# Optimization experiments

Hardware: AMD Instinct MI355X
Metric: run time of the kernel (lower is better)

Reference implementation:

```python
import jax, jax.numpy as jnp
import numpy as np
import math

D_MODEL = 1024
NUM_HEADS = 16
D_K = D_MODEL // NUM_HEADS
THETA = 10000.0
BATCH = 2
SEQ = 2048


def _trunc_normal(key, shape, std):
    # truncated normal in [-3std, 3std], matching torch.nn.init.trunc_normal_
    return jax.random.truncated_normal(key, -3.0, 3.0, shape, jnp.float32) * std


def setup_inputs() -> dict:
    key = jax.random.key(0)
    kx, kq, kk, kv, ko = jax.random.split(key, 5)
    std = math.sqrt(2.0 / (D_MODEL + D_MODEL))
    return {
        "x": jax.random.normal(kx, (BATCH, SEQ, D_MODEL), jnp.float32),
        "Wq": _trunc_normal(kq, (D_MODEL, D_MODEL), std),
        "Wk": _trunc_normal(kk, (D_MODEL, D_MODEL), std),
        "Wv": _trunc_normal(kv, (D_MODEL, D_MODEL), std),
        "Wo": _trunc_normal(ko, (D_MODEL, D_MODEL), std),
    }


def _apply_rope(t):
    # t: [B, H, S, d_k]; positions = arange(S)
    S = t.shape[-2]
    inv_freq = 1.0 / THETA ** (jnp.arange(0, D_K, 2, dtype=jnp.float32) / D_K)
    ang = jnp.arange(S, dtype=jnp.float32)[:, None] * inv_freq[None, :]  # [S, d_k/2]
    cos, sin = jnp.cos(ang), jnp.sin(ang)
    t1 = t[..., ::2]
    t2 = t[..., 1::2]
    r1 = t1 * cos - t2 * sin
    r2 = t1 * sin + t2 * cos
    # interleave back: even indices <- r1, odd <- r2
    out = jnp.stack([r1, r2], axis=-1).reshape(t.shape)
    return out


def reference(x, Wq, Wk, Wv, Wo):
    B, S, _ = x.shape
    def proj(W):
        return (x @ W.T).reshape(B, S, NUM_HEADS, D_K).transpose(0, 2, 1, 3)
    q = _apply_rope(proj(Wq))
    k = _apply_rope(proj(Wk))
    v = proj(Wv)
    scores = jnp.einsum('bhqd,bhkd->bhqk', q, k) / math.sqrt(D_K)
    causal = jnp.tril(jnp.ones((S, S), dtype=bool))
    scores = jnp.where(causal, scores, -jnp.inf)
    attn = jax.nn.softmax(scores, axis=-1)
    ctx = jnp.einsum('bhqk,bhkd->bhqd', attn, v)  # [B,H,S,d_k]
    ctx = ctx.transpose(0, 2, 1, 3).reshape(B, S, D_MODEL)
    return ctx @ Wo.T
```

## Files before the change

### kernel.cpp

```cpp
#include <hip/hip_runtime.h>
#include <hip/hip_bf16.h>


typedef __attribute__((ext_vector_type(8))) short bf16x8;
typedef __attribute__((ext_vector_type(4))) short bf16x4;
typedef __attribute__((ext_vector_type(4))) float f32x4;

#define D_MODEL 1024
#define SEQ     2048
#define NHEAD   16
#define DK      64
#define EXP_BIAS 16.0f

__device__ __forceinline__ f32x4 mfma16(bf16x8 a, bf16x8 b, f32x4 c) {
    return __builtin_amdgcn_mfma_f32_16x16x32_bf16(a, b, c, 0, 0, 0);
}

__device__ __forceinline__ void load_lds16(const __hip_bfloat16* g, __hip_bfloat16* l) {
    __builtin_amdgcn_global_load_lds((const __attribute__((address_space(1))) void*)g,
                                     (__attribute__((address_space(3))) void*)l,
                                     16, 0, 0);
}

__device__ __forceinline__ void cvt8(const float* p, __hip_bfloat16* dst) {
    const float4 f0 = *(const float4*)p;
    const float4 f1 = *(const float4*)(p + 4);
    alignas(16) __hip_bfloat16 t[8] = {
        __float2bfloat16(f0.x), __float2bfloat16(f0.y),
        __float2bfloat16(f0.z), __float2bfloat16(f0.w),
        __float2bfloat16(f1.x), __float2bfloat16(f1.y),
        __float2bfloat16(f1.z), __float2bfloat16(f1.w)};
    *(bf16x8*)dst = *(const bf16x8*)t;
}

__global__ __launch_bounds__(256) void cvt5_k(const float* __restrict__ wq,
                                              const float* __restrict__ wk,
                                              const float* __restrict__ wv,
                                              const float* __restrict__ wo,
                                              const float* __restrict__ x,
                                              __hip_bfloat16* __restrict__ dw,
                                              __hip_bfloat16* __restrict__ dwo,
                                              __hip_bfloat16* __restrict__ dx) {
    const int id = blockIdx.x;
    const float* s;
    __hip_bfloat16* d;
    int off;
    if (id < 1536)      { const int w = id >> 9; s = (w == 0) ? wq : (w == 1 ? wk : wv);
                          d = dw + (size_t)w * 1024 * 1024; off = (id & 511) * 2048; }
    else if (id < 2048) { s = wo; d = dwo; off = (id - 1536) * 2048; }
    else                { s = x;  d = dx;  off = (id - 2048) * 2048; }
    const int i = off + threadIdx.x * 8;
    alignas(16) __hip_bfloat16 t[8];
    cvt8(s + i, t);
    *(bf16x8*)(d + i) = *(const bf16x8*)t;
}

__global__ __launch_bounds__(256) void cvt3_k(const float* __restrict__ s0,
                                              const float* __restrict__ s1,
                                              const float* __restrict__ s2,
                                              __hip_bfloat16* __restrict__ d0,
                                              __hip_bfloat16* __restrict__ d1,
                                              __hip_bfloat16* __restrict__ d2) {
    const float* s = (blockIdx.y == 0) ? s0 : (blockIdx.y == 1 ? s1 : s2);
    __hip_bfloat16* d = (blockIdx.y == 0) ? d0 : (blockIdx.y == 1 ? d1 : d2);
    const int i = (blockIdx.x * 256 + threadIdx.x) * 8;
    alignas(16) __hip_bfloat16 t[8];
    cvt8(s + i, t);
    *(bf16x8*)(d + i) = *(const bf16x8*)t;
}

__device__ __forceinline__ void qkv_epilogue(f32x4 (&acc)[4][4], int wsel,
                                             int bm, int bn, int wave,
                                             int quad, int l15,
                                             __hip_bfloat16* Cq,
                                             __hip_bfloat16* Ck,
                                             __hip_bfloat16* Vt) {
    if (wsel < 2) {
        __hip_bfloat16* C = (wsel == 0) ? Cq : Ck;
#pragma unroll
        for (int i = 0; i < 4; ++i)
#pragma unroll
            for (int j = 0; j < 4; ++j)
#pragma unroll
                for (int r = 0; r < 4; ++r) {
                    const int row = bm + (wave >> 1) * 64 + i * 16 + quad * 4 + r;
                    const int col = bn + (wave & 1) * 64 + j * 16 + l15;
                    C[(size_t)row * 1024 + col] = __float2bfloat16(acc[i][j][r]);
                }
    } else {
#pragma unroll
        for (int i = 0; i < 4; ++i)
#pragma unroll
            for (int j = 0; j < 4; ++j) {
                const int col  = bn + (wave & 1) * 64 + j * 16 + l15;
                const int hh   = col >> 6, dd = col & 63;
                const int row0 = bm + (wave >> 1) * 64 + i * 16 + quad * 4;
                const int bb   = row0 >> 11, s0 = row0 & 2047;
                alignas(8) __hip_bfloat16 t4[4] = {
                    __float2bfloat16(acc[i][j][0]), __float2bfloat16(acc[i][j][1]),
                    __float2bfloat16(acc[i][j][2]), __float2bfloat16(acc[i][j][3])};
                *(uint2*)&Vt[((size_t)(bb * 16 + hh) * 64 + dd) * 2048 + s0] =
                    *(const uint2*)t4;
            }
    }
}

__global__ __launch_bounds__(256) void gemm_qkv_bf(const __hip_bfloat16* __restrict__ X,
                                                   const __hip_bfloat16* __restrict__ W,
                                                   __hip_bfloat16* __restrict__ Cq,
                                                   __hip_bfloat16* __restrict__ Ck,
                                                   __hip_bfloat16* __restrict__ Vt) {
    __shared__ alignas(16) __hip_bfloat16 a_lds[128 * 32];
    __shared__ alignas(16) __hip_bfloat16 b_lds[128 * 32];

    const int tid  = threadIdx.x;
    const int wave = tid >> 6;
    const int lane = tid & 63;
    const int quad = lane >> 4;
    const int l15  = lane & 15;

    const int wsel = blockIdx.x >> 3;
    const int bn   = (blockIdx.x & 7) * 128;
    const int bm   = blockIdx.y * 128;

    const __hip_bfloat16* B = W + (size_t)wsel * 1024 * 1024;

    f32x4 acc[4][4] = {};

    for (int k0 = 0; k0 < 1024; k0 += 32) {
        __syncthreads();
#pragma unroll
        for (int c = 0; c < 2; ++c) {
            const int chunk = (wave * 2 + c) * 64 + lane;
            const int row = chunk >> 2;
            const int col = (chunk & 3) * 8;
            load_lds16(&X[(size_t)(bm + row) * 1024 + k0 + col],
                       &a_lds[(wave * 2 + c) * 512]);
            load_lds16(&B[(size_t)(bn + row) * 1024 + k0 + col],
                       &b_lds[(wave * 2 + c) * 512]);
        }
        __syncthreads();

        bf16x8 af[4], bfr[4];
#pragma unroll
        for (int i = 0; i < 4; ++i)
            af[i] = *(const bf16x8*)&a_lds[((wave >> 1) * 64 + i * 16 + l15) * 32 + quad * 8];
#pragma unroll
        for (int j = 0; j < 4; ++j)
            bfr[j] = *(const bf16x8*)&b_lds[((wave & 1) * 64 + j * 16 + l15) * 32 + quad * 8];
#pragma unroll
        for (int i = 0; i < 4; ++i)
#pragma unroll
            for (int j = 0; j < 4; ++j)
                acc[i][j] = mfma16(af[i], bfr[j], acc[i][j]);
    }

    qkv_epilogue(acc, wsel, bm, bn, wave, quad, l15, Cq, Ck, Vt);
}

__global__ __launch_bounds__(256) void gemm_qkv_f32(const float* __restrict__ X,
                                                    const __hip_bfloat16* __restrict__ W,
                                                    __hip_bfloat16* __restrict__ Cq,
                                                    __hip_bfloat16* __restrict__ Ck,
                                                    __hip_bfloat16* __restrict__ Vt) {
    __shared__ alignas(16) __hip_bfloat16 a_lds[128 * 32];
    __shared__ alignas(16) __hip_bfloat16 b_lds[128 * 32];

    const int tid  = threadIdx.x;
    const int wave = tid >> 6;
    const int lane = tid & 63;
    const int quad = lane >> 4;
    const int l15  = lane & 15;

    const int wsel = blockIdx.x >> 3;
    const int bn   = (blockIdx.x & 7) * 128;
    const int bm   = blockIdx.y * 128;

    const __hip_bfloat16* B = W + (size_t)wsel * 1024 * 1024;

    f32x4 acc[4][4] = {};

    for (int k0 = 0; k0 < 1024; k0 += 32) {
        __syncthreads();
#pragma unroll
        for (int c = 0; c < 2; ++c) {
            const int e   = (c * 256 + tid) * 8;
            const int row = e >> 5;
            const int col = e & 31;
            cvt8(&X[(size_t)(bm + row) * 1024 + k0 + col], &a_lds[e]);
        }
#pragma unroll
        for (int c = 0; c < 2; ++c) {
            const int chunk = (wave * 2 + c) * 64 + lane;
            const int row = chunk >> 2;
            const int col = (chunk & 3) * 8;
            load_lds16(&B[(size_t)(bn + row) * 1024 + k0 + col],
                       &b_lds[(wave * 2 + c) * 512]);
        }
        __syncthreads();

        bf16x8 af[4], bfr[4];
#pragma unroll
        for (int i = 0; i < 4; ++i)
            af[i] = *(const bf16x8*)&a_lds[((wave >> 1) * 64 + i * 16 + l15) * 32 + quad * 8];
#pragma unroll
        for (int j = 0; j < 4; ++j)
            bfr[j] = *(const bf16x8*)&b_lds[((wave & 1) * 64 + j * 16 + l15) * 32 + quad * 8];
#pragma unroll
        for (int i = 0; i < 4; ++i)
#pragma unroll
            for (int j = 0; j < 4; ++j)
                acc[i][j] = mfma16(af[i], bfr[j], acc[i][j]);
    }

    qkv_epilogue(acc, wsel, bm, bn, wave, quad, l15, Cq, Ck, Vt);
}

__global__ __launch_bounds__(128) void gemm_o(const __hip_bfloat16* __restrict__ A,
                                              const __hip_bfloat16* __restrict__ B,
                                              float* __restrict__ C) {
    __shared__ alignas(16) __hip_bfloat16 a_lds[128 * 32];
    __shared__ alignas(16) __hip_bfloat16 b_lds[64 * 32];

    const int tid  = threadIdx.x;
    const int wave = tid >> 6;
    const int lane = tid & 63;
    const int quad = lane >> 4;
    const int l15  = lane & 15;

    const int bn = blockIdx.x * 64;
    const int bm = blockIdx.y * 128;

    f32x4 acc[4][4] = {};

    for (int k0 = 0; k0 < 1024; k0 += 32) {
        __syncthreads();
#pragma unroll
        for (int c = 0; c < 4; ++c) {
            const int chunk = (wave * 4 + c) * 64 + lane;
            const int row = chunk >> 2;
            const int col = (chunk & 3) * 8;
            load_lds16(&A[(size_t)(bm + row) * 1024 + k0 + col],
                       &a_lds[(wave * 4 + c) * 512]);
        }
#pragma unroll
        for (int c = 0; c < 2; ++c) {
            const int chunk = (wave * 2 + c) * 64 + lane;
            const int row = chunk >> 2;
            const int col = (chunk & 3) * 8;
            load_lds16(&B[(size_t)(bn + row) * 1024 + k0 + col],
                       &b_lds[(wave * 2 + c) * 512]);
        }
        __syncthreads();

        bf16x8 af[4], bfr[4];
#pragma unroll
        for (int i = 0; i < 4; ++i)
            af[i] = *(const bf16x8*)&a_lds[(wave * 64 + i * 16 + l15) * 32 + quad * 8];
#pragma unroll
        for (int j = 0; j < 4; ++j)
            bfr[j] = *(const bf16x8*)&b_lds[(j * 16 + l15) * 32 + quad * 8];
#pragma unroll
        for (int i = 0; i < 4; ++i)
#pragma unroll
            for (int j = 0; j < 4; ++j)
                acc[i][j] = mfma16(af[i], bfr[j], acc[i][j]);
    }

#pragma unroll
    for (int i = 0; i < 4; ++i)
#pragma unroll
        for (int j = 0; j < 4; ++j)
#pragma unroll
            for (int r = 0; r < 4; ++r) {
                const int row = bm + wave * 64 + i * 16 + quad * 4 + r;
                const int col = bn + j * 16 + l15;
                C[(size_t)row * 1024 + col] = acc[i][j][r];
            }
}

__global__ __launch_bounds__(256) void rope_k(__hip_bfloat16* Q, __hip_bfloat16* K) {
    const int idx = blockIdx.x * 256 + threadIdx.x;
    const int row = idx >> 7;
    const int g   = idx & 127;
    const int col = g * 8;
    const int s   = row & (SEQ - 1);
    const int i0  = (g & 7) * 4;

    float sn[4], cs[4];
#pragma unroll
    for (int z = 0; z < 4; ++z) {
        const float ang = (float)s * __expf(-(float)(i0 + z) * 0.28782313663f);
        __sincosf(ang, &sn[z], &cs[z]);
    }

    const size_t o = (size_t)row * D_MODEL + col;
    alignas(16) __hip_bfloat16 q8[8], k8[8];
    *(uint4*)q8 = *(const uint4*)&Q[o];
    *(uint4*)k8 = *(const uint4*)&K[o];
#pragma unroll
    for (int z = 0; z < 4; ++z) {
        const float q1 = __bfloat162float(q8[2 * z]);
        const float q2 = __bfloat162float(q8[2 * z + 1]);
        q8[2 * z]     = __float2bfloat16((q1 * cs[z] - q2 * sn[z]) * 0.125f);
        q8[2 * z + 1] = __float2bfloat16((q1 * sn[z] + q2 * cs[z]) * 0.125f);
        const float k1 = __bfloat162float(k8[2 * z]);
        const float k2 = __bfloat162float(k8[2 * z + 1]);
        k8[2 * z]     = __float2bfloat16(k1 * cs[z] - k2 * sn[z]);
        k8[2 * z + 1] = __float2bfloat16(k1 * sn[z] + k2 * cs[z]);
    }
    *(uint4*)&Q[o] = *(const uint4*)q8;
    *(uint4*)&K[o] = *(const uint4*)k8;
}

__global__ __launch_bounds__(256, 4) void attn_k(const __hip_bfloat16* Q,
                                                 const __hip_bfloat16* K,
                                                 const __hip_bfloat16* Vt,
                                                 __hip_bfloat16* O) {
    __shared__ alignas(16) __hip_bfloat16 k_s[2][64 * 72];
    __shared__ alignas(16) __hip_bfloat16 vt_s[2][64 * 72];

    const int tid  = threadIdx.x;
    const int wave = tid >> 6;
    const int lane = tid & 63;
    const int quad = lane >> 4;
    const int l15  = lane & 15;

    const int hw = blockIdx.x;
    const int j  = hw >> 3;
    const int g  = j >> 5;
    const int m  = j & 31;
    const int bh = (hw & 7) * 4 + g;
    const int mm = (g >= 2) ? ((m + 8) & 31) : m;
    const int qt = (g & 1) ? mm : (31 - mm);
    const int b  = bh >> 4;
    const int h  = bh & 15;
    const int q0 = qt * 64;

    const int r0 = tid >> 3;
    const int d8 = (tid & 7) * 8;
    const int vp0 = ((d8 >> 5) << 5) + (((d8 & 15) >> 2) << 3) + (((d8 >> 4) & 1) << 2);
    const int d4  = d8 + 4;
    const int vp1 = ((d4 >> 5) << 5) + (((d4 & 15) >> 2) << 3) + (((d4 >> 4) & 1) << 2);

    const size_t vtBase = (size_t)bh * (64 * 2048);
    const size_t baseK0 = ((size_t)(b * SEQ)) * D_MODEL + h * DK;

#pragma unroll
    for (int c = 0; c < 2; ++c) {
        const int row = r0 + c * 32;
        const uint4 kv = *(const uint4*)&K[baseK0 + (size_t)row * D_MODEL + d8];
        const uint4 vv = *(const uint4*)&Vt[vtBase + (size_t)row * 2048 + d8];
        *(uint4*)&k_s[0][row * 72 + d8] = kv;
        uint2 lo, hi;
        lo.x = vv.x; lo.y = vv.y; hi.x = vv.z; hi.y = vv.w;
        *(uint2*)&vt_s[0][row * 72 + vp0] = lo;
        *(uint2*)&vt_s[0][row * 72 + vp1] = hi;
    }

    bf16x8 qa0, qa1;
    {
        const size_t baseQ = ((size_t)(b * SEQ + q0 + wave * 16 + l15)) * D_MODEL + h * DK;
        qa0 = *(const bf16x8*)&Q[baseQ + quad * 8];
        qa1 = *(const bf16x8*)&Q[baseQ + 32 + quad * 8];
    }
    __syncthreads();

    float l4[4] = {0.f, 0.f, 0.f, 0.f};
    f32x4 o_acc[4] = {};

    for (int kt = 0; kt < qt; ++kt) {
        const int buf = kt & 1;

        uint4 kr0, kr1, vr0, vr1;
        {
            const size_t baseK = baseK0 + (size_t)(kt + 1) * 64 * D_MODEL;
            const size_t baseV = vtBase + (size_t)(kt + 1) * 64;
            kr0 = *(const uint4*)&K[baseK + (size_t)r0 * D_MODEL + d8];
            kr1 = *(const uint4*)&K[baseK + (size_t)(r0 + 32) * D_MODEL + d8];
            vr0 = *(const uint4*)&Vt[baseV + (size_t)r0 * 2048 + d8];
            vr1 = *(const uint4*)&Vt[baseV + (size_t)(r0 + 32) * 2048 + d8];
        }

        alignas(16) __hip_bfloat16 pk0[8], pk1[8];
#pragma unroll
        for (int t = 0; t < 4; ++t) {
            __hip_bfloat16* dst = (t < 2) ? pk0 : pk1;
            const int zo = (t & 1) * 4;
            f32x4 a = {};
            const bf16x8 kb0 = *(const bf16x8*)&k_s[buf][(t * 16 + l15) * 72 + quad * 8];
            a = mfma16(kb0, qa0, a);
            const bf16x8 kb1 = *(const bf16x8*)&k_s[buf][(t * 16 + l15) * 72 + 32 + quad * 8];
            a = mfma16(kb1, qa1, a);
#pragma unroll
            for (int r = 0; r < 4; ++r) {
                const float pv = __expf(a[r] - EXP_BIAS);
                l4[r] += pv;
                dst[zo + r] = __float2bfloat16(pv);
            }
        }
        const bf16x8 pa0 = *(const bf16x8*)pk0;
        const bf16x8 pa1 = *(const bf16x8*)pk1;

#pragma unroll
        for (int ks = 0; ks < 2; ++ks) {
            const bf16x8 pa = ks ? pa1 : pa0;
#pragma unroll
            for (int t2 = 0; t2 < 4; ++t2) {
                const bf16x8 vv = *(const bf16x8*)
                    &vt_s[buf][(t2 * 16 + l15) * 72 + ks * 32 + quad * 8];
                o_acc[t2] = mfma16(pa, vv, o_acc[t2]);
            }
        }

        *(uint4*)&k_s[buf ^ 1][r0 * 72 + d8] = kr0;
        *(uint4*)&k_s[buf ^ 1][(r0 + 32) * 72 + d8] = kr1;
        {
            uint2 lo0, hi0, lo1, hi1;
            lo0.x = vr0.x; lo0.y = vr0.y; hi0.x = vr0.z; hi0.y = vr0.w;
            lo1.x = vr1.x; lo1.y = vr1.y; hi1.x = vr1.z; hi1.y = vr1.w;
            *(uint2*)&vt_s[buf ^ 1][r0 * 72 + vp0] = lo0;
            *(uint2*)&vt_s[buf ^ 1][r0 * 72 + vp1] = hi0;
            *(uint2*)&vt_s[buf ^ 1][(r0 + 32) * 72 + vp0] = lo1;
            *(uint2*)&vt_s[buf ^ 1][(r0 + 32) * 72 + vp1] = hi1;
        }

        __syncthreads();
    }

    {
        const int buf = qt & 1;
        alignas(16) __hip_bfloat16 pk0[8], pk1[8];
#pragma unroll
        for (int t = 0; t < 4; ++t) {
            __hip_bfloat16* dst = (t < 2) ? pk0 : pk1;
            const int zo = (t & 1) * 4;
            if (t > wave) {
#pragma unroll
                for (int r = 0; r < 4; ++r) dst[zo + r] = __float2bfloat16(0.0f);
                continue;
            }
            f32x4 a = {};
            const bf16x8 kb0 = *(const bf16x8*)&k_s[buf][(t * 16 + l15) * 72 + quad * 8];
            a = mfma16(kb0, qa0, a);
            const bf16x8 kb1 = *(const bf16x8*)&k_s[buf][(t * 16 + l15) * 72 + 32 + quad * 8];
            a = mfma16(kb1, qa1, a);
#pragma unroll
            for (int r = 0; r < 4; ++r) {
                float v = a[r];
                if (t == wave && (quad * 4 + r > l15)) v = -1e30f;
                const float pv = __expf(v - EXP_BIAS);
                l4[r] += pv;
                dst[zo + r] = __float2bfloat16(pv);
            }
        }
        const bf16x8 pa0 = *(const bf16x8*)pk0;
        const bf16x8 pa1 = *(const bf16x8*)pk1;

#pragma unroll
        for (int ks = 0; ks < 2; ++ks) {
            if (ks == 1 && wave < 2) continue;
            const bf16x8 pa = ks ? pa1 : pa0;
#pragma unroll
            for (int t2 = 0; t2 < 4; ++t2) {
                const bf16x8 vv = *(const bf16x8*)
                    &vt_s[buf][(t2 * 16 + l15) * 72 + ks * 32 + quad * 8];
                o_acc[t2] = mfma16(pa, vv, o_acc[t2]);
            }
        }
    }

    float l_loc = (l4[0] + l4[1]) + (l4[2] + l4[3]);
    l_loc += __shfl_xor(l_loc, 16);
    l_loc += __shfl_xor(l_loc, 32);
    float lr[4];
#pragma unroll
    for (int r = 0; r < 4; ++r) lr[r] = __shfl(l_loc, quad * 4 + r);

#pragma unroll
    for (int t2 = 0; t2 < 4; ++t2)
#pragma unroll
        for (int r = 0; r < 4; ++r) {
            const int row = q0 + wave * 16 + quad * 4 + r;
            const int d   = t2 * 16 + l15;
            O[((size_t)(b * SEQ + row)) * D_MODEL + h * DK + d] =
                __float2bfloat16(o_acc[t2][r] / lr[r]);
        }
}

extern "C" void kernel_launch(void* const* d_in, const int* in_sizes, int n_in,
                              void* d_out, int out_size, void* d_ws, size_t ws_size,
                              hipStream_t stream) {
    const float* x  = (const float*)d_in[0];
    const float* Wq = (const float*)d_in[1];
    const float* Wk = (const float*)d_in[2];
    const float* Wv = (const float*)d_in[3];
    const float* Wo = (const float*)d_in[4];

    const size_t MT = (size_t)4096 * 1024;
    const size_t WT = (size_t)1024 * 1024;
    __hip_bfloat16* Qw = (__hip_bfloat16*)d_ws;
    __hip_bfloat16* Vt = Qw + MT;
    __hip_bfloat16* Wb = (__hip_bfloat16*)d_out;
    __hip_bfloat16* Kw = (__hip_bfloat16*)((char*)d_out + 8 * 1024 * 1024);

    const bool big = ws_size >= (size_t)26 * 1024 * 1024;

    if (big) {
        __hip_bfloat16* xb  = Qw + 2 * MT;
        __hip_bfloat16* WoB = (__hip_bfloat16*)((char*)d_ws + 24 * 1024 * 1024);
        cvt5_k<<<4096, 256, 0, stream>>>(Wq, Wk, Wv, Wo, x, Wb, WoB, xb);
        gemm_qkv_bf<<<dim3(24, 32), 256, 0, stream>>>(xb, Wb, Qw, Kw, Vt);
        rope_k<<<(4096 * 128) / 256, 256, 0, stream>>>(Qw, Kw);
        attn_k<<<dim3(1024), 256, 0, stream>>>(Qw, Kw, Vt, Qw);
        gemm_o<<<dim3(16, 32), 128, 0, stream>>>(Qw, WoB, (float*)d_out);
    } else {
        __hip_bfloat16* WoB = Vt;
        cvt3_k<<<dim3(512, 3), 256, 0, stream>>>(Wq, Wk, Wv, Wb, Wb + WT, Wb + 2 * WT);
        gemm_qkv_f32<<<dim3(24, 32), 256, 0, stream>>>(x, Wb, Qw, Kw, Vt);
        rope_k<<<(4096 * 128) / 256, 256, 0, stream>>>(Qw, Kw);
        attn_k<<<dim3(1024), 256, 0, stream>>>(Qw, Kw, Vt, Qw);
        cvt3_k<<<dim3(512, 1), 256, 0, stream>>>(Wo, Wo, Wo, WoB, WoB, WoB);
        gemm_o<<<dim3(16, 32), 128, 0, stream>>>(Qw, WoB, (float*)d_out);
    }
}
```

Measured before the change: 181.9 us.

## Fuse RoPE into QKV epilogue, double-buffer GEMMs, widen gemm_o, set MFMA priority

RoPE and the Q scaling move into the QKV GEMM epilogue, computing sin/cos per element and using a lane shuffle to fetch the paired value. This removes the separate rope kernel and its read/write pass over Q and K. The QKV and output GEMMs switch to double-buffered LDS staging with a single barrier per k-step, and gemm_o goes to 256 threads with each wave owning 32 rows. The attention loop raises wave priority around its MFMA sections; the trade-off is more transcendental math and shuffles in the epilogue and higher LDS use.

```diff
diff --git a/kernel.cpp b/kernel.cpp
--- a/kernel.cpp
+++ b/kernel.cpp
@@ -11,6 +11,7 @@
 #define NHEAD   16
 #define DK      64
 #define EXP_BIAS 16.0f
+#define ROPE_LN 0.28782313663f
 
 __device__ __forceinline__ f32x4 mfma16(bf16x8 a, bf16x8 b, f32x4 c) {
     return __builtin_amdgcn_mfma_f32_16x16x32_bf16(a, b, c, 0, 0, 0);
@@ -77,16 +78,27 @@
                                              __hip_bfloat16* Vt) {
     if (wsel < 2) {
         __hip_bfloat16* C = (wsel == 0) ? Cq : Ck;
-#pragma unroll
-        for (int i = 0; i < 4; ++i)
-#pragma unroll
-            for (int j = 0; j < 4; ++j)
+        const float qscale = (wsel == 0) ? 0.125f : 1.0f;
+        const float sgn = (l15 & 1) ? 1.0f : -1.0f;
+#pragma unroll
+        for (int j = 0; j < 4; ++j) {
+            const int ipair = (j * 16 + l15) >> 1;
+            const float invf = __expf(-(float)ipair * ROPE_LN);
+            const int col = bn + (wave & 1) * 64 + j * 16 + l15;
+#pragma unroll
+            for (int i = 0; i < 4; ++i)
 #pragma unroll
                 for (int r = 0; r < 4; ++r) {
                     const int row = bm + (wave >> 1) * 64 + i * 16 + quad * 4 + r;
-                    const int col = bn + (wave & 1) * 64 + j * 16 + l15;
-                    C[(size_t)row * 1024 + col] = __float2bfloat16(acc[i][j][r]);
+                    const int s = row & (SEQ - 1);
+                    float sn, cs;
+                    __sincosf((float)s * invf, &sn, &cs);
+                    const float v = acc[i][j][r];
+                    const float part = __shfl_xor(v, 1);
+                    const float out = (v * cs + part * (sgn * sn)) * qscale;
+                    C[(size_t)row * 1024 + col] = __float2bfloat16(out);
                 }
+        }
     } else {
 #pragma unroll
         for (int i = 0; i < 4; ++i)
@@ -110,8 +122,8 @@
                                                    __hip_bfloat16* __restrict__ Cq,
                                                    __hip_bfloat16* __restrict__ Ck,
                                                    __hip_bfloat16* __restrict__ Vt) {
-    __shared__ alignas(16) __hip_bfloat16 a_lds[128 * 32];
-    __shared__ alignas(16) __hip_bfloat16 b_lds[128 * 32];
+    __shared__ alignas(16) __hip_bfloat16 a_lds[2][128 * 32];
+    __shared__ alignas(16) __hip_bfloat16 b_lds[2][128 * 32];
 
     const int tid  = threadIdx.x;
     const int wave = tid >> 6;
@@ -127,32 +139,40 @@
 
     f32x4 acc[4][4] = {};
 
-    for (int k0 = 0; k0 < 1024; k0 += 32) {
-        __syncthreads();
+    auto stage = [&](int buf, int k0) {
 #pragma unroll
         for (int c = 0; c < 2; ++c) {
             const int chunk = (wave * 2 + c) * 64 + lane;
             const int row = chunk >> 2;
             const int col = (chunk & 3) * 8;
             load_lds16(&X[(size_t)(bm + row) * 1024 + k0 + col],
-                       &a_lds[(wave * 2 + c) * 512]);
+                       &a_lds[buf][(wave * 2 + c) * 512]);
             load_lds16(&B[(size_t)(bn + row) * 1024 + k0 + col],
-                       &b_lds[(wave * 2 + c) * 512]);
-        }
-        __syncthreads();
+                       &b_lds[buf][(wave * 2 + c) * 512]);
+        }
+    };
+
+    stage(0, 0);
+    __syncthreads();
+
+    for (int k0 = 0; k0 < 1024; k0 += 32) {
+        const int buf = (k0 >> 5) & 1;
+        if (k0 + 32 < 1024) stage(buf ^ 1, k0 + 32);
 
         bf16x8 af[4], bfr[4];
 #pragma unroll
         for (int i = 0; i < 4; ++i)
-            af[i] = *(const bf16x8*)&a_lds[((wave >> 1) * 64 + i * 16 + l15) * 32 + quad * 8];
+            af[i] = *(const bf16x8*)&a_lds[buf][((wave >> 1) * 64 + i * 16 + l15) * 32 + quad * 8];
 #pragma unroll
         for (int j = 0; j < 4; ++j)
-            bfr[j] = *(const bf16x8*)&b_lds[((wave & 1) * 64 + j * 16 + l15) * 32 + quad * 8];
+            bfr[j] = *(const bf16x8*)&b_lds[buf][((wave & 1) * 64 + j * 16 + l15) * 32 + quad * 8];
 #pragma unroll
         for (int i = 0; i < 4; ++i)
 #pragma unroll
             for (int j = 0; j < 4; ++j)
                 acc[i][j] = mfma16(af[i], bfr[j], acc[i][j]);
+
+        __syncthreads();
     }
 
     qkv_epilogue(acc, wsel, bm, bn, wave, quad, l15, Cq, Ck, Vt);
@@ -216,11 +236,11 @@
     qkv_epilogue(acc, wsel, bm, bn, wave, quad, l15, Cq, Ck, Vt);
 }
 
-__global__ __launch_bounds__(128) void gemm_o(const __hip_bfloat16* __restrict__ A,
+__global__ __launch_bounds__(256) void gemm_o(const __hip_bfloat16* __restrict__ A,
                                               const __hip_bfloat16* __restrict__ B,
                                               float* __restrict__ C) {
-    __shared__ alignas(16) __hip_bfloat16 a_lds[128 * 32];
-    __shared__ alignas(16) __hip_bfloat16 b_lds[64 * 32];
+    __shared__ alignas(16) __hip_bfloat16 a_lds[2][128 * 32];
+    __shared__ alignas(16) __hip_bfloat16 b_lds[2][64 * 32];
 
     const int tid  = threadIdx.x;
     const int wave = tid >> 6;
@@ -231,86 +251,59 @@
     const int bn = blockIdx.x * 64;
     const int bm = blockIdx.y * 128;
 
-    f32x4 acc[4][4] = {};
-
-    for (int k0 = 0; k0 < 1024; k0 += 32) {
-        __syncthreads();
-#pragma unroll
-        for (int c = 0; c < 4; ++c) {
-            const int chunk = (wave * 4 + c) * 64 + lane;
-            const int row = chunk >> 2;
-            const int col = (chunk & 3) * 8;
-            load_lds16(&A[(size_t)(bm + row) * 1024 + k0 + col],
-                       &a_lds[(wave * 4 + c) * 512]);
-        }
+    f32x4 acc[2][4] = {};
+
+    auto stage = [&](int buf, int k0) {
 #pragma unroll
         for (int c = 0; c < 2; ++c) {
             const int chunk = (wave * 2 + c) * 64 + lane;
             const int row = chunk >> 2;
             const int col = (chunk & 3) * 8;
+            load_lds16(&A[(size_t)(bm + row) * 1024 + k0 + col],
+                       &a_lds[buf][(wave * 2 + c) * 512]);
+        }
+        {
+            const int chunk = wave * 64 + lane;
+            const int row = chunk >> 2;
+            const int col = (chunk & 3) * 8;
             load_lds16(&B[(size_t)(bn + row) * 1024 + k0 + col],
-                       &b_lds[(wave * 2 + c) * 512]);
-        }
-        __syncthreads();
-
-        bf16x8 af[4], bfr[4];
-#pragma unroll
-        for (int i = 0; i < 4; ++i)
-            af[i] = *(const bf16x8*)&a_lds[(wave * 64 + i * 16 + l15) * 32 + quad * 8];
+                       &b_lds[buf][wave * 512]);
+        }
+    };
+
+    stage(0, 0);
+    __syncthreads();
+
+    for (int k0 = 0; k0 < 1024; k0 += 32) {
+        const int buf = (k0 >> 5) & 1;
+        if (k0 + 32 < 1024) stage(buf ^ 1, k0 + 32);
+
+        bf16x8 af[2], bfr[4];
+#pragma unroll
+        for (int i = 0; i < 2; ++i)
+            af[i] = *(const bf16x8*)&a_lds[buf][(wave * 32 + i * 16 + l15) * 32 + quad * 8];
 #pragma unroll
         for (int j = 0; j < 4; ++j)
-            bfr[j] = *(const bf16x8*)&b_lds[(j * 16 + l15) * 32 + quad * 8];
-#pragma unroll
-        for (int i = 0; i < 4; ++i)
+            bfr[j] = *(const bf16x8*)&b_lds[buf][(j * 16 + l15) * 32 + quad * 8];
+#pragma unroll
+        for (int i = 0; i < 2; ++i)
 #pragma unroll
             for (int j = 0; j < 4; ++j)
                 acc[i][j] = mfma16(af[i], bfr[j], acc[i][j]);
-    }
-
-#pragma unroll
-    for (int i = 0; i < 4; ++i)
+
+        __syncthreads();
+    }
+
+#pragma unroll
+    for (int i = 0; i < 2; ++i)
 #pragma unroll
         for (int j = 0; j < 4; ++j)
 #pragma unroll
             for (int r = 0; r < 4; ++r) {
-                const int row = bm + wave * 64 + i * 16 + quad * 4 + r;
+                const int row = bm + wave * 32 + i * 16 + quad * 4 + r;
                 const int col = bn + j * 16 + l15;
                 C[(size_t)row * 1024 + col] = acc[i][j][r];
             }
-}
-
-__global__ __launch_bounds__(256) void rope_k(__hip_bfloat16* Q, __hip_bfloat16* K) {
-    const int idx = blockIdx.x * 256 + threadIdx.x;
-    const int row = idx >> 7;
-    const int g   = idx & 127;
-    const int col = g * 8;
-    const int s   = row & (SEQ - 1);
-    const int i0  = (g & 7) * 4;
-
-    float sn[4], cs[4];
-#pragma unroll
-    for (int z = 0; z < 4; ++z) {
-        const float ang = (float)s * __expf(-(float)(i0 + z) * 0.28782313663f);
-        __sincosf(ang, &sn[z], &cs[z]);
-    }
-
-    const size_t o = (size_t)row * D_MODEL + col;
-    alignas(16) __hip_bfloat16 q8[8], k8[8];
-    *(uint4*)q8 = *(const uint4*)&Q[o];
-    *(uint4*)k8 = *(const uint4*)&K[o];
-#pragma unroll
-    for (int z = 0; z < 4; ++z) {
-        const float q1 = __bfloat162float(q8[2 * z]);
-        const float q2 = __bfloat162float(q8[2 * z + 1]);
-        q8[2 * z]     = __float2bfloat16((q1 * cs[z] - q2 * sn[z]) * 0.125f);
-        q8[2 * z + 1] = __float2bfloat16((q1 * sn[z] + q2 * cs[z]) * 0.125f);
-        const float k1 = __bfloat162float(k8[2 * z]);
-        const float k2 = __bfloat162float(k8[2 * z + 1]);
-        k8[2 * z]     = __float2bfloat16(k1 * cs[z] - k2 * sn[z]);
-        k8[2 * z + 1] = __float2bfloat16(k1 * sn[z] + k2 * cs[z]);
-    }
-    *(uint4*)&Q[o] = *(const uint4*)q8;
-    *(uint4*)&K[o] = *(const uint4*)k8;
 }
 
 __global__ __launch_bounds__(256, 4) void attn_k(const __hip_bfloat16* Q,
@@ -388,10 +381,12 @@
             __hip_bfloat16* dst = (t < 2) ? pk0 : pk1;
             const int zo = (t & 1) * 4;
             f32x4 a = {};
+            __builtin_amdgcn_s_setprio(1);
             const bf16x8 kb0 = *(const bf16x8*)&k_s[buf][(t * 16 + l15) * 72 + quad * 8];
             a = mfma16(kb0, qa0, a);
             const bf16x8 kb1 = *(const bf16x8*)&k_s[buf][(t * 16 + l15) * 72 + 32 + quad * 8];
             a = mfma16(kb1, qa1, a);
+            __builtin_amdgcn_s_setprio(0);
 #pragma unroll
             for (int r = 0; r < 4; ++r) {
                 const float pv = __expf(a[r] - EXP_BIAS);
@@ -402,6 +397,7 @@
         const bf16x8 pa0 = *(const bf16x8*)pk0;
         const bf16x8 pa1 = *(const bf16x8*)pk1;
 
+        __builtin_amdgcn_s_setprio(1);
 #pragma unroll
         for (int ks = 0; ks < 2; ++ks) {
             const bf16x8 pa = ks ? pa1 : pa0;
@@ -412,6 +408,7 @@
                 o_acc[t2] = mfma16(pa, vv, o_acc[t2]);
             }
         }
+        __builtin_amdgcn_s_setprio(0);
 
         *(uint4*)&k_s[buf ^ 1][r0 * 72 + d8] = kr0;
         *(uint4*)&k_s[buf ^ 1][(r0 + 32) * 72 + d8] = kr1;
@@ -511,16 +508,14 @@
         __hip_bfloat16* WoB = (__hip_bfloat16*)((char*)d_ws + 24 * 1024 * 1024);
         cvt5_k<<<4096, 256, 0, stream>>>(Wq, Wk, Wv, Wo, x, Wb, WoB, xb);
         gemm_qkv_bf<<<dim3(24, 32), 256, 0, stream>>>(xb, Wb, Qw, Kw, Vt);
-        rope_k<<<(4096 * 128) / 256, 256, 0, stream>>>(Qw, Kw);
         attn_k<<<dim3(1024), 256, 0, stream>>>(Qw, Kw, Vt, Qw);
-        gemm_o<<<dim3(16, 32), 128, 0, stream>>>(Qw, WoB, (float*)d_out);
+        gemm_o<<<dim3(16, 32), 256, 0, stream>>>(Qw, WoB, (float*)d_out);
     } else {
         __hip_bfloat16* WoB = Vt;
         cvt3_k<<<dim3(512, 3), 256, 0, stream>>>(Wq, Wk, Wv, Wb, Wb + WT, Wb + 2 * WT);
         gemm_qkv_f32<<<dim3(24, 32), 256, 0, stream>>>(x, Wb, Qw, Kw, Vt);
-        rope_k<<<(4096 * 128) / 256, 256, 0, stream>>>(Qw, Kw);
         attn_k<<<dim3(1024), 256, 0, stream>>>(Qw, Kw, Vt, Qw);
         cvt3_k<<<dim3(512, 1), 256, 0, stream>>>(Wo, Wo, Wo, WoB, WoB, WoB);
-        gemm_o<<<dim3(16, 32), 128, 0, stream>>>(Qw, WoB, (float*)d_out);
-    }
-}
+        gemm_o<<<dim3(16, 32), 256, 0, stream>>>(Qw, WoB, (float*)d_out);
+    }
+}
```

After: 192.1 us. 5.6% more time.

## Double-buffer output GEMM with four waves, use exp2 and setprio in attention

Applied to the files above, without the earlier changes.

The output projection GEMM moves from two to four waves per block, each wave owning 32 rows, and double-buffers its LDS tiles so the next k-slice's global-to-LDS loads are issued before the current slice's MFMAs, leaving one barrier per iteration. In attention, the biased exp becomes a single fma plus native exp2 with the bias folded into the log2 domain. s_setprio raises wave priority around the MFMA blocks. Together these aim to hide load latency in gemm_o and trim VALU work in the softmax, at the cost of doubled LDS in gemm_o and fewer accumulators per wave.

```diff
diff --git a/kernel.cpp b/kernel.cpp
--- a/kernel.cpp
+++ b/kernel.cpp
@@ -10,10 +10,15 @@
 #define SEQ     2048
 #define NHEAD   16
 #define DK      64
-#define EXP_BIAS 16.0f
+#define LOG2E   1.4426950408889634f
+#define EXPB2   23.083120654223414f
 
 __device__ __forceinline__ f32x4 mfma16(bf16x8 a, bf16x8 b, f32x4 c) {
     return __builtin_amdgcn_mfma_f32_16x16x32_bf16(a, b, c, 0, 0, 0);
+}
+
+__device__ __forceinline__ float expm16(float a) {
+    return __builtin_amdgcn_exp2f(__builtin_fmaf(a, LOG2E, -EXPB2));
 }
 
 __device__ __forceinline__ void load_lds16(const __hip_bfloat16* g, __hip_bfloat16* l) {
@@ -216,11 +221,11 @@
     qkv_epilogue(acc, wsel, bm, bn, wave, quad, l15, Cq, Ck, Vt);
 }
 
-__global__ __launch_bounds__(128) void gemm_o(const __hip_bfloat16* __restrict__ A,
+__global__ __launch_bounds__(256) void gemm_o(const __hip_bfloat16* __restrict__ A,
                                               const __hip_bfloat16* __restrict__ B,
                                               float* __restrict__ C) {
-    __shared__ alignas(16) __hip_bfloat16 a_lds[128 * 32];
-    __shared__ alignas(16) __hip_bfloat16 b_lds[64 * 32];
+    __shared__ alignas(16) __hip_bfloat16 a_lds[2][128 * 32];
+    __shared__ alignas(16) __hip_bfloat16 b_lds[2][64 * 32];
 
     const int tid  = threadIdx.x;
     const int wave = tid >> 6;
@@ -231,49 +236,56 @@
     const int bn = blockIdx.x * 64;
     const int bm = blockIdx.y * 128;
 
-    f32x4 acc[4][4] = {};
-
-    for (int k0 = 0; k0 < 1024; k0 += 32) {
-        __syncthreads();
-#pragma unroll
-        for (int c = 0; c < 4; ++c) {
-            const int chunk = (wave * 4 + c) * 64 + lane;
-            const int row = chunk >> 2;
-            const int col = (chunk & 3) * 8;
-            load_lds16(&A[(size_t)(bm + row) * 1024 + k0 + col],
-                       &a_lds[(wave * 4 + c) * 512]);
-        }
+    f32x4 acc[2][4] = {};
+
+    auto stage = [&](int buf, int k0) {
 #pragma unroll
         for (int c = 0; c < 2; ++c) {
             const int chunk = (wave * 2 + c) * 64 + lane;
             const int row = chunk >> 2;
             const int col = (chunk & 3) * 8;
+            load_lds16(&A[(size_t)(bm + row) * 1024 + k0 + col],
+                       &a_lds[buf][(wave * 2 + c) * 512]);
+        }
+        {
+            const int chunk = wave * 64 + lane;
+            const int row = chunk >> 2;
+            const int col = (chunk & 3) * 8;
             load_lds16(&B[(size_t)(bn + row) * 1024 + k0 + col],
-                       &b_lds[(wave * 2 + c) * 512]);
-        }
-        __syncthreads();
-
-        bf16x8 af[4], bfr[4];
-#pragma unroll
-        for (int i = 0; i < 4; ++i)
-            af[i] = *(const bf16x8*)&a_lds[(wave * 64 + i * 16 + l15) * 32 + quad * 8];
+                       &b_lds[buf][wave * 512]);
+        }
+    };
+
+    stage(0, 0);
+    __syncthreads();
+
+    for (int k0 = 0; k0 < 1024; k0 += 32) {
+        const int buf = (k0 >> 5) & 1;
+        if (k0 + 32 < 1024) stage(buf ^ 1, k0 + 32);
+
+        bf16x8 af[2], bfr[4];
+#pragma unroll
+        for (int i = 0; i < 2; ++i)
+            af[i] = *(const bf16x8*)&a_lds[buf][(wave * 32 + i * 16 + l15) * 32 + quad * 8];
 #pragma unroll
         for (int j = 0; j < 4; ++j)
-            bfr[j] = *(const bf16x8*)&b_lds[(j * 16 + l15) * 32 + quad * 8];
-#pragma unroll
-        for (int i = 0; i < 4; ++i)
+            bfr[j] = *(const bf16x8*)&b_lds[buf][(j * 16 + l15) * 32 + quad * 8];
+#pragma unroll
+        for (int i = 0; i < 2; ++i)
 #pragma unroll
             for (int j = 0; j < 4; ++j)
                 acc[i][j] = mfma16(af[i], bfr[j], acc[i][j]);
-    }
-
-#pragma unroll
-    for (int i = 0; i < 4; ++i)
+
+        __syncthreads();
+    }
+
+#pragma unroll
+    for (int i = 0; i < 2; ++i)
 #pragma unroll
         for (int j = 0; j < 4; ++j)
 #pragma unroll
             for (int r = 0; r < 4; ++r) {
-                const int row = bm + wave * 64 + i * 16 + quad * 4 + r;
+                const int row = bm + wave * 32 + i * 16 + quad * 4 + r;
                 const int col = bn + j * 16 + l15;
                 C[(size_t)row * 1024 + col] = acc[i][j][r];
             }
@@ -388,13 +400,15 @@
             __hip_bfloat16* dst = (t < 2) ? pk0 : pk1;
             const int zo = (t & 1) * 4;
             f32x4 a = {};
+            __builtin_amdgcn_s_setprio(1);
             const bf16x8 kb0 = *(const bf16x8*)&k_s[buf][(t * 16 + l15) * 72 + quad * 8];
             a = mfma16(kb0, qa0, a);
             const bf16x8 kb1 = *(const bf16x8*)&k_s[buf][(t * 16 + l15) * 72 + 32 + quad * 8];
             a = mfma16(kb1, qa1, a);
+            __builtin_amdgcn_s_setprio(0);
 #pragma unroll
             for (int r = 0; r < 4; ++r) {
-                const float pv = __expf(a[r] - EXP_BIAS);
+                const float pv = expm16(a[r]);
                 l4[r] += pv;
                 dst[zo + r] = __float2bfloat16(pv);
             }
@@ -402,6 +416,7 @@
         const bf16x8 pa0 = *(const bf16x8*)pk0;
         const bf16x8 pa1 = *(const bf16x8*)pk1;
 
+        __builtin_amdgcn_s_setprio(1);
 #pragma unroll
         for (int ks = 0; ks < 2; ++ks) {
             const bf16x8 pa = ks ? pa1 : pa0;
@@ -412,6 +427,7 @@
                 o_acc[t2] = mfma16(pa, vv, o_acc[t2]);
             }
         }
+        __builtin_amdgcn_s_setprio(0);
 
         *(uint4*)&k_s[buf ^ 1][r0 * 72 + d8] = kr0;
         *(uint4*)&k_s[buf ^ 1][(r0 + 32) * 72 + d8] = kr1;
@@ -449,7 +465,7 @@
             for (int r = 0; r < 4; ++r) {
                 float v = a[r];
                 if (t == wave && (quad * 4 + r > l15)) v = -1e30f;
-                const float pv = __expf(v - EXP_BIAS);
+                const float pv = expm16(v);
                 l4[r] += pv;
                 dst[zo + r] = __float2bfloat16(pv);
             }
@@ -513,7 +529,7 @@
         gemm_qkv_bf<<<dim3(24, 32), 256, 0, stream>>>(xb, Wb, Qw, Kw, Vt);
         rope_k<<<(4096 * 128) / 256, 256, 0, stream>>>(Qw, Kw);
         attn_k<<<dim3(1024), 256, 0, stream>>>(Qw, Kw, Vt, Qw);
-        gemm_o<<<dim3(16, 32), 128, 0, stream>>>(Qw, WoB, (float*)d_out);
+        gemm_o<<<dim3(16, 32), 256, 0, stream>>>(Qw, WoB, (float*)d_out);
     } else {
         __hip_bfloat16* WoB = Vt;
         cvt3_k<<<dim3(512, 3), 256, 0, stream>>>(Wq, Wk, Wv, Wb, Wb + WT, Wb + 2 * WT);
@@ -521,6 +537,6 @@
         rope_k<<<(4096 * 128) / 256, 256, 0, stream>>>(Qw, Kw);
         attn_k<<<dim3(1024), 256, 0, stream>>>(Qw, Kw, Vt, Qw);
         cvt3_k<<<dim3(512, 1), 256, 0, stream>>>(Wo, Wo, Wo, WoB, WoB, WoB);
-        gemm_o<<<dim3(16, 32), 128, 0, stream>>>(Qw, WoB, (float*)d_out);
-    }
-}
+        gemm_o<<<dim3(16, 32), 256, 0, stream>>>(Qw, WoB, (float*)d_out);
+    }
+}
```

New measurement: 185.0 us. About the same (+1.7%).
